# Kernel optimization log

Hardware: AMD Instinct MI355X
Metric: run time of the kernel (lower is better)

Reference implementation:

```python
import jax, jax.numpy as jnp
import numpy as np

B, T, D, NW, NC, S, L, H, FF = 32, 128, 512, 2000, 200, 8, 4, 8, 2048
HD = D // H


def layer_norm(x, g, b, eps=1e-5):
    m = jnp.mean(x, -1, keepdims=True)
    v = jnp.var(x, -1, keepdims=True)
    return (x - m) * jax.lax.rsqrt(v + eps) * g + b


def mha(x, Wq, bq, Wk, bk, Wv, bv, Wo, bo):
    b_, t_, d_ = x.shape
    q = (x @ Wq + bq).reshape(b_, t_, H, HD)
    k = (x @ Wk + bk).reshape(b_, t_, H, HD)
    v = (x @ Wv + bv).reshape(b_, t_, H, HD)
    s = jnp.einsum('bqhd,bkhd->bhqk', q, k) / np.float32(np.sqrt(HD))
    a = jax.nn.softmax(s, -1)
    o = jnp.einsum('bhqk,bkhd->bqhd', a, v).reshape(b_, t_, d_)
    return o @ Wo + bo


def conv1d(x, w, b):  # x [B,C,T], w [O,I,3], same padding
    y = jax.lax.conv_general_dilated(x, w, (1,), [(1, 1)], dimension_numbers=('NCH', 'OIH', 'NCH'))
    return y + b[None, :, None]


def setup_inputs() -> dict:
    key = jax.random.key(0)
    ks = jax.random.split(key, 48)
    n = lambda k, shape, s=0.02: jax.random.normal(k, shape, jnp.float32) * s
    inp = {}
    inp['vid_feats'] = jax.random.normal(ks[0], (B, T, D), jnp.float32)
    inp['segs_feats'] = jax.random.normal(ks[1], (B, S, D), jnp.float32)
    inp['actn_feats'] = jax.random.normal(ks[2], (NC, D), jnp.float32)
    inp['actn_concepts'] = jax.random.normal(ks[3], (NW, D), jnp.float32)
    inp['pos_enc'] = n(ks[4], (1, T, D))
    # TemporalTransformer (L stacked encoder layers, post-norm, relu FFN)
    inp['tf_Wq'] = n(ks[5], (L, D, D)); inp['tf_bq'] = jnp.zeros((L, D), jnp.float32)
    inp['tf_Wk'] = n(ks[6], (L, D, D)); inp['tf_bk'] = jnp.zeros((L, D), jnp.float32)
    inp['tf_Wv'] = n(ks[7], (L, D, D)); inp['tf_bv'] = jnp.zeros((L, D), jnp.float32)
    inp['tf_Wo'] = n(ks[8], (L, D, D)); inp['tf_bo'] = jnp.zeros((L, D), jnp.float32)
    inp['tf_W1'] = n(ks[9], (L, D, FF)); inp['tf_b1'] = jnp.zeros((L, FF), jnp.float32)
    inp['tf_W2'] = n(ks[10], (L, FF, D)); inp['tf_b2'] = jnp.zeros((L, D), jnp.float32)
    inp['tf_ln1_g'] = jnp.ones((L, D), jnp.float32); inp['tf_ln1_b'] = jnp.zeros((L, D), jnp.float32)
    inp['tf_ln2_g'] = jnp.ones((L, D), jnp.float32); inp['tf_ln2_b'] = jnp.zeros((L, D), jnp.float32)
    # AttentionProjectionModule (out_proj is defined but unused in its forward)
    inp['pq_W'] = n(ks[11], (D, D)); inp['pq_b'] = jnp.zeros((D,), jnp.float32)
    inp['pk_W'] = n(ks[12], (D, D)); inp['pk_b'] = jnp.zeros((D,), jnp.float32)
    inp['pv_W'] = n(ks[13], (D, D)); inp['pv_b'] = jnp.zeros((D,), jnp.float32)
    # temp_conv stack 2000->1024->512->256->128->1, k=3, pad=1
    inp['c1_w'] = n(ks[14], (1024, NW, 3)); inp['c1_b'] = jnp.zeros((1024,), jnp.float32)
    inp['c2_w'] = n(ks[15], (512, 1024, 3)); inp['c2_b'] = jnp.zeros((512,), jnp.float32)
    inp['c3_w'] = n(ks[16], (256, 512, 3)); inp['c3_b'] = jnp.zeros((256,), jnp.float32)
    inp['c4_w'] = n(ks[17], (128, 256, 3)); inp['c4_b'] = jnp.zeros((128,), jnp.float32)
    inp['c5_w'] = n(ks[18], (1, 128, 3)); inp['c5_b'] = jnp.zeros((1,), jnp.float32)
    # ragged segments: inclusive [start, end] per the torch stf:edf+1 slicing
    st = jax.random.randint(ks[19], (B, S), 0, T - 16)
    ln = jax.random.randint(ks[20], (B, S), 0, 16)
    ed = jnp.minimum(st + ln, T - 1)
    inp['seg_steds'] = jnp.stack([st, ed], -1).astype(jnp.int32)  # [B,S,2]
    return inp


def reference(vid_feats, segs_feats, actn_feats, actn_concepts, pos_enc,
              tf_Wq, tf_bq, tf_Wk, tf_bk, tf_Wv, tf_bv, tf_Wo, tf_bo,
              tf_W1, tf_b1, tf_W2, tf_b2, tf_ln1_g, tf_ln1_b, tf_ln2_g, tf_ln2_b,
              pq_W, pq_b, pk_W, pk_b, pv_W, pv_b,
              c1_w, c1_b, c2_w, c2_b, c3_w, c3_b, c4_w, c4_b, c5_w, c5_b,
              seg_steds):
    # --- TemporalTransformer ---
    x = vid_feats + pos_enc
    for l in range(L):
        x = layer_norm(x + mha(x, tf_Wq[l], tf_bq[l], tf_Wk[l], tf_bk[l], tf_Wv[l], tf_bv[l], tf_Wo[l], tf_bo[l]), tf_ln1_g[l], tf_ln1_b[l])
        ff = jax.nn.relu(x @ tf_W1[l] + tf_b1[l]) @ tf_W2[l] + tf_b2[l]
        x = layer_norm(x + ff, tf_ln2_g[l], tf_ln2_b[l])
    vid_feats_proj = vid_feats + x  # [B,T,D]
    # --- AttentionProjectionModule (words attend to video frames) ---
    wf = jax.lax.stop_gradient(actn_concepts)  # detached concept table [NW,D]
    Q = (wf @ pq_W + pq_b).reshape(NW, H, HD)  # shared across batch
    K = (vid_feats_proj @ pk_W + pk_b).reshape(B, T, H, HD)
    V = (vid_feats_proj @ pv_W + pv_b).reshape(B, T, H, HD)
    s = jnp.einsum('nhd,bthd->bhnt', Q, K) / np.float32(np.sqrt(HD))
    a = jax.nn.softmax(s, -1)
    upd = jnp.einsum('bhnt,bthd->bnhd', a, V).reshape(B, NW, D)
    feats_proj = jnp.einsum('btd,bnd->btn', vid_feats_proj, upd)  # [B,T,NW]
    # --- temp_conv + sigmoid ---
    h = feats_proj.transpose(0, 2, 1)  # [B,NW,T]
    h = jax.nn.relu(conv1d(h, c1_w, c1_b))
    h = jax.nn.relu(conv1d(h, c2_w, c2_b))
    h = jax.nn.relu(conv1d(h, c3_w, c3_b))
    h = jax.nn.relu(conv1d(h, c4_w, c4_b))
    frames_cls = jax.nn.sigmoid(conv1d(h, c5_w, c5_b))  # [B,1,T]
    weights = frames_cls[:, 0, :]  # [B,T]
    # --- ragged per-segment softmax-weighted sum pooling (mask-vectorized) ---
    t_idx = jnp.arange(T)
    st = seg_steds[..., 0]; ed = seg_steds[..., 1]  # [B,S]
    mask = (t_idx[None, None, :] >= st[..., None]) & (t_idx[None, None, :] <= ed[..., None])  # [B,S,T]
    scores = jnp.where(mask, weights[:, None, :], -1e30)
    w = jax.nn.softmax(scores, -1)  # per-segment softmax over frames in segment
    seg_feats = jnp.einsum('bst,btd->bsd', w, vid_feats)  # [B,S,D]
    actn_logits = jnp.einsum('bsd,cd->bsc', seg_feats, jax.lax.stop_gradient(actn_feats))  # [B,S,NC]
    return frames_cls, actn_logits, feats_proj
```

## Files before the change

### kernel.cpp

```cpp
#include <hip/hip_runtime.h>
#include <hip/hip_bf16.h>

#define BB 32
#define TT 128
#define DD 512
#define NW 2000
#define NCC 200
#define SS 8
#define LL 4
#define HH 8
#define FF 2048
#define HD 64

typedef unsigned short ushort_t;
typedef __attribute__((ext_vector_type(8))) short bhalf8;
typedef __attribute__((ext_vector_type(4))) float floatx4;

__device__ inline ushort_t f2b(float x) {
    union { float f; unsigned int u; } v; v.f = x;
    unsigned int r = (v.u + 0x7FFFu + ((v.u >> 16) & 1u)) >> 16;
    return (ushort_t)r;
}
__device__ inline float b2f(ushort_t u) {
    union { unsigned int u; float f; } v; v.u = ((unsigned int)u) << 16;
    return v.f;
}
__device__ inline void gld16(const ushort_t* g, ushort_t* l) {
    __builtin_amdgcn_global_load_lds(
        (const __attribute__((address_space(1))) void*)g,
        (__attribute__((address_space(3))) void*)l, 16, 0, 0);
}

template<int ACT, int OUTBF>
__global__ __launch_bounds__(256) void bgemm_k(
    const ushort_t* __restrict__ A, int lda, long sA1, long sA2,
    const ushort_t* __restrict__ B, int ldb, long sB1, long sB2,
    void* __restrict__ Cv, int ldc, long sC1, long sC2,
    const float* __restrict__ bias,
    int M, int N, int K, float alpha, int batchH,
    int taps, long tapA, long tapB, const ushort_t* __restrict__ zbuf)
{
    __shared__ __align__(16) ushort_t sm[2][2][128 * 64];
    int z = blockIdx.z;
    int zb = z / batchH, zh = z % batchH;
    A += (long)zb * sA1 + (long)zh * sA2;
    B += (long)zb * sB1 + (long)zh * sB2;
    long cOff = (long)zb * sC1 + (long)zh * sC2;
    int m0 = blockIdx.y * 128, n0 = blockIdx.x * 128;
    int tid = threadIdx.x;
    int wid = tid >> 6, lane = tid & 63;
    int wr = wid >> 1, wc = wid & 1;
    int lr = lane & 15, lg = lane >> 4;

    int kSteps = (K + 63) >> 6;
    int nt = taps * kSteps;

    int rsub = lane >> 3;
    int ssub = lane & 7;
    int scol = ((ssub ^ rsub) << 3);
    bool aok[4], bok[4];
    const ushort_t* aptr[4];
    const ushort_t* bptr[4];
    #pragma unroll
    for (int i = 0; i < 4; i++) {
        int row = (wid << 5) + (i << 3) + rsub;
        aok[i] = (m0 + row) < M;
        bok[i] = (n0 + row) < N;
        aptr[i] = A + (long)(m0 + row) * lda + scol;
        bptr[i] = B + (long)(n0 + row) * ldb + scol;
    }

    floatx4 acc[4][4];
    #pragma unroll
    for (int i = 0; i < 4; i++)
        #pragma unroll
        for (int j = 0; j < 4; j++)
            acc[i][j] = (floatx4){0.f, 0.f, 0.f, 0.f};

    {
        bool kOk = scol < K;
        #pragma unroll
        for (int i = 0; i < 4; i++) {
            const ushort_t* as = (kOk && aok[i]) ? aptr[i] : zbuf;
            const ushort_t* bs = (kOk && bok[i]) ? bptr[i] : zbuf;
            int lb = ((wid << 5) + (i << 3)) << 6;
            gld16(as, &sm[0][0][lb]);
            gld16(bs, &sm[0][1][lb]);
        }
    }
    __syncthreads();

    int cur = 0;
    int tap_n = 0, k0_n = 0;
    for (int t = 0; t < nt; t++) {
        k0_n += 64;
        if (k0_n >= K) { k0_n = 0; ++tap_n; }
        if (tap_n < taps) {
            bool kOk = (k0_n + scol) < K;
            #pragma unroll
            for (int i = 0; i < 4; i++) {
                const ushort_t* as =
                    (kOk && aok[i]) ? (aptr[i] + (long)tap_n * tapA + k0_n) : zbuf;
                const ushort_t* bs =
                    (kOk && bok[i]) ? (bptr[i] + (long)tap_n * tapB + k0_n) : zbuf;
                int lb = ((wid << 5) + (i << 3)) << 6;
                gld16(as, &sm[cur ^ 1][0][lb]);
                gld16(bs, &sm[cur ^ 1][1][lb]);
            }
        }
        const char* Ab = (const char*)&sm[cur][0][0];
        const char* Bbs = (const char*)&sm[cur][1][0];
        #pragma unroll
        for (int kk = 0; kk < 2; kk++) {
            bhalf8 a_[4], b_[4];
            #pragma unroll
            for (int i = 0; i < 4; i++) {
                int r = wr * 64 + i * 16 + lr;
                int off = (r << 7) + (((kk << 6) + (lg << 4)) ^ ((r & 7) << 4));
                a_[i] = *(const bhalf8*)(Ab + off);
            }
            #pragma unroll
            for (int j = 0; j < 4; j++) {
                int r = wc * 64 + j * 16 + lr;
                int off = (r << 7) + (((kk << 6) + (lg << 4)) ^ ((r & 7) << 4));
                b_[j] = *(const bhalf8*)(Bbs + off);
            }
            #pragma unroll
            for (int i = 0; i < 4; i++)
                #pragma unroll
                for (int j = 0; j < 4; j++)
                    acc[i][j] = __builtin_amdgcn_mfma_f32_16x16x32_bf16(
                        a_[i], b_[j], acc[i][j], 0, 0, 0);
        }
        __syncthreads();
        cur ^= 1;
    }

    #pragma unroll
    for (int i = 0; i < 4; i++) {
        int gm_base = m0 + wr * 64 + i * 16 + lg * 4;
        #pragma unroll
        for (int j = 0; j < 4; j++) {
            int gn = n0 + wc * 64 + j * 16 + lr;
            if (gn >= N) continue;
            float bv = bias ? bias[gn] : 0.f;
            #pragma unroll
            for (int r = 0; r < 4; r++) {
                int gm = gm_base + r;
                if (gm >= M) continue;
                float v = acc[i][j][r] * alpha + bv;
                if (ACT == 1) v = fmaxf(v, 0.f);
                long idx = cOff + (long)gm * ldc + gn;
                if (OUTBF) ((ushort_t*)Cv)[idx] = f2b(v);
                else       ((float*)Cv)[idx] = v;
            }
        }
    }
}

static void launch_bgemm(int act, int outbf,
                         const ushort_t* A, int lda, long sA1, long sA2,
                         const ushort_t* B, int ldb, long sB1, long sB2,
                         void* C, int ldc, long sC1, long sC2,
                         const float* bias, int M, int N, int K, float alpha,
                         int batchH, int Z, int taps, long tapA, long tapB,
                         const ushort_t* zbuf, hipStream_t st) {
    dim3 grid((N + 127) / 128, (M + 127) / 128, Z), blk(256);
#define BG(A_, O_) bgemm_k<A_, O_><<<grid, blk, 0, st>>>(A, lda, sA1, sA2, B, ldb, sB1, sB2, C, ldc, sC1, sC2, bias, M, N, K, alpha, batchH, taps, tapA, tapB, zbuf)
    if (act) { if (outbf) BG(1, 1); else BG(1, 0); }
    else     { if (outbf) BG(0, 1); else BG(0, 0); }
#undef BG
}

template<int CHECKQ>
__global__ __launch_bounds__(256) void fattn_k(
    const ushort_t* __restrict__ Q, int ldq, long sQb, long sQc,
    const ushort_t* __restrict__ K, int ldk, long sKb,
    const ushort_t* __restrict__ VT, long sVb,
    ushort_t* __restrict__ O, int ldo, long sOb, long sOc,
    int nc, int Mtot, const ushort_t* __restrict__ zbuf)
{
    __shared__ __align__(16) ushort_t Qs[128 * 64];
    __shared__ __align__(16) ushort_t Ks[128 * 64];
    __shared__ __align__(16) ushort_t Vs[64 * 128];
    __shared__ __align__(16) ushort_t Ps[128 * 128];
    int z = blockIdx.x;
    int c = z % nc, rr_ = z / nc;
    int h = rr_ % HH, b = rr_ / HH;
    int mQ = Mtot - c * 128;
    const ushort_t* Qb = Q + (long)b * sQb + (long)c * sQc + h * 64;
    const ushort_t* Kb = K + (long)b * sKb + h * 64;
    const ushort_t* Vb = VT + (long)b * sVb + (long)h * 64 * 128;
    ushort_t* Ob = O + (long)b * sOb + (long)c * sOc + h * 64;

    int tid = threadIdx.x, wid = tid >> 6, lane = tid & 63;
    int lr = lane & 15, lg = lane >> 4;

    {
        int rsub = lane >> 3, csub = lane & 7;
        #pragma unroll
        for (int i = 0; i < 4; i++) {
            int row = wid * 32 + i * 8 + rsub;
            int cc = (csub ^ rsub) * 8;
            const ushort_t* qs = (!CHECKQ || row < mQ) ? (Qb + (long)row * ldq + cc) : zbuf;
            gld16(qs, &Qs[(wid * 32 + i * 8) * 64]);
            gld16(Kb + (long)row * ldk + cc, &Ks[(wid * 32 + i * 8) * 64]);
        }
        int d4 = lane >> 4, c16 = lane & 15;
        #pragma unroll
        for (int i = 0; i < 4; i++) {
            int d = wid * 16 + i * 4 + d4;
            int cc = (c16 ^ (d & 7)) * 8;
            gld16(Vb + (long)d * 128 + cc, &Vs[(wid * 16 + i * 4) * 128]);
        }
    }
    __syncthreads();

    floatx4 acc[2][8];
    #pragma unroll
    for (int i = 0; i < 2; i++)
        #pragma unroll
        for (int j = 0; j < 8; j++)
            acc[i][j] = (floatx4){0.f, 0.f, 0.f, 0.f};
    const char* Qc = (const char*)Qs;
    const char* Kc = (const char*)Ks;
    #pragma unroll
    for (int kk = 0; kk < 2; kk++) {
        bhalf8 a_[2], b_[8];
        #pragma unroll
        for (int i = 0; i < 2; i++) {
            int r = wid * 32 + i * 16 + lr;
            a_[i] = *(const bhalf8*)(Qc + (r << 7) + ((((kk << 2) + lg) ^ (r & 7)) << 4));
        }
        #pragma unroll
        for (int j = 0; j < 8; j++) {
            int r = j * 16 + lr;
            b_[j] = *(const bhalf8*)(Kc + (r << 7) + ((((kk << 2) + lg) ^ (r & 7)) << 4));
        }
        #pragma unroll
        for (int i = 0; i < 2; i++)
            #pragma unroll
            for (int j = 0; j < 8; j++)
                acc[i][j] = __builtin_amdgcn_mfma_f32_16x16x32_bf16(
                    a_[i], b_[j], acc[i][j], 0, 0, 0);
    }

    #pragma unroll
    for (int i = 0; i < 2; i++) {
        #pragma unroll
        for (int r = 0; r < 4; r++) {
            int row = wid * 32 + i * 16 + lg * 4 + r;
            float v[8], m = -1e30f;
            #pragma unroll
            for (int j = 0; j < 8; j++) { v[j] = acc[i][j][r] * 0.125f; m = fmaxf(m, v[j]); }
            #pragma unroll
            for (int o = 8; o > 0; o >>= 1) m = fmaxf(m, __shfl_xor(m, o, 64));
            float s = 0.f;
            #pragma unroll
            for (int j = 0; j < 8; j++) { v[j] = expf(v[j] - m); s += v[j]; }
            #pragma unroll
            for (int o = 8; o > 0; o >>= 1) s += __shfl_xor(s, o, 64);
            float inv = 1.f / s;
            #pragma unroll
            for (int j = 0; j < 8; j++) {
                int col = j * 16 + lr;
                int byte = (row << 8) + ((((col >> 3) ^ (row & 7)) << 4)) + ((col & 7) << 1);
                *(ushort_t*)((char*)Ps + byte) = f2b(v[j] * inv);
            }
        }
    }
    __syncthreads();

    floatx4 acc2[2][4];
    #pragma unroll
    for (int i = 0; i < 2; i++)
        #pragma unroll
        for (int j = 0; j < 4; j++)
            acc2[i][j] = (floatx4){0.f, 0.f, 0.f, 0.f};
    const char* Pc = (const char*)Ps;
    const char* Vc = (const char*)Vs;
    #pragma unroll
    for (int kk = 0; kk < 4; kk++) {
        bhalf8 a_[2], b_[4];
        #pragma unroll
        for (int i = 0; i < 2; i++) {
            int r = wid * 32 + i * 16 + lr;
            a_[i] = *(const bhalf8*)(Pc + (r << 8) + ((((kk << 2) + lg) ^ (r & 7)) << 4));
        }
        #pragma unroll
        for (int j = 0; j < 4; j++) {
            int d = j * 16 + lr;
            b_[j] = *(const bhalf8*)(Vc + (d << 8) + ((((kk << 2) + lg) ^ (d & 7)) << 4));
        }
        #pragma unroll
        for (int i = 0; i < 2; i++)
            #pragma unroll
            for (int j = 0; j < 4; j++)
                acc2[i][j] = __builtin_amdgcn_mfma_f32_16x16x32_bf16(
                    a_[i], b_[j], acc2[i][j], 0, 0, 0);
    }
    #pragma unroll
    for (int i = 0; i < 2; i++) {
        #pragma unroll
        for (int r = 0; r < 4; r++) {
            int q = wid * 32 + i * 16 + lg * 4 + r;
            if (CHECKQ && q >= mQ) continue;
            #pragma unroll
            for (int j = 0; j < 4; j++) {
                int d = j * 16 + lr;
                Ob[(long)q * ldo + d] = f2b(acc2[i][j][r]);
            }
        }
    }
}

template<int TRANSB>
__global__ __launch_bounds__(256) void gemm_k(
    const float* __restrict__ A, int lda,
    const float* __restrict__ B, int ldb,
    float* __restrict__ C, int ldc,
    int M, int N, int K)
{
    __shared__ float As[16][68];
    __shared__ float Bs[16][68];
    int m0 = blockIdx.y * 64, n0 = blockIdx.x * 64;
    int tid = threadIdx.x;
    int tr = tid / 16, tc = tid % 16;
    float acc[4][4] = {};
    for (int k0 = 0; k0 < K; k0 += 16) {
        {
            int ar = tid / 4;
            int ac = (tid % 4) * 4;
            int gm = m0 + ar;
            #pragma unroll
            for (int i = 0; i < 4; i++) {
                int gk = k0 + ac + i;
                As[ac + i][ar] = (gm < M && gk < K) ? A[(long)gm * lda + gk] : 0.f;
            }
        }
        {
            int bn = tid / 4;
            int bk = (tid % 4) * 4;
            int gn = n0 + bn;
            #pragma unroll
            for (int i = 0; i < 4; i++) {
                int gk = k0 + bk + i;
                Bs[bk + i][bn] = (gn < N && gk < K) ? B[(long)gn * ldb + gk] : 0.f;
            }
        }
        __syncthreads();
        #pragma unroll
        for (int kk = 0; kk < 16; kk++) {
            float a[4], b[4];
            #pragma unroll
            for (int i = 0; i < 4; i++) a[i] = As[kk][tr * 4 + i];
            #pragma unroll
            for (int i = 0; i < 4; i++) b[i] = Bs[kk][tc * 4 + i];
            #pragma unroll
            for (int i = 0; i < 4; i++)
                #pragma unroll
                for (int j = 0; j < 4; j++)
                    acc[i][j] += a[i] * b[j];
        }
        __syncthreads();
    }
    #pragma unroll
    for (int i = 0; i < 4; i++) {
        int gm = m0 + tr * 4 + i;
        if (gm >= M) continue;
        #pragma unroll
        for (int j = 0; j < 4; j++) {
            int gn = n0 + tc * 4 + j;
            if (gn >= N) continue;
            C[(long)gm * ldc + gn] = acc[i][j];
        }
    }
}

__global__ void f2b_k(const float* __restrict__ in, ushort_t* __restrict__ out, long n) {
    long stride = (long)gridDim.x * blockDim.x * 8;
    for (long i = ((long)blockIdx.x * blockDim.x + threadIdx.x) * 8; i < n; i += stride) {
        float4 a = *(const float4*)(in + i);
        float4 b = *(const float4*)(in + i + 4);
        uint4 o;
        o.x = (unsigned)f2b(a.x) | ((unsigned)f2b(a.y) << 16);
        o.y = (unsigned)f2b(a.z) | ((unsigned)f2b(a.w) << 16);
        o.z = (unsigned)f2b(b.x) | ((unsigned)f2b(b.y) << 16);
        o.w = (unsigned)f2b(b.z) | ((unsigned)f2b(b.w) << 16);
        *(uint4*)(out + i) = o;
    }
}
__global__ void add_f2b_k(const float* __restrict__ a, const float* __restrict__ b,
                          ushort_t* __restrict__ out, long n) {
    long stride = (long)gridDim.x * blockDim.x * 8;
    for (long i = ((long)blockIdx.x * blockDim.x + threadIdx.x) * 8; i < n; i += stride) {
        float4 x = *(const float4*)(a + i);
        float4 y = *(const float4*)(b + i);
        float4 x2 = *(const float4*)(a + i + 4);
        float4 y2 = *(const float4*)(b + i + 4);
        uint4 o;
        o.x = (unsigned)f2b(x.x + y.x) | ((unsigned)f2b(x.y + y.y) << 16);
        o.y = (unsigned)f2b(x.z + y.z) | ((unsigned)f2b(x.w + y.w) << 16);
        o.z = (unsigned)f2b(x2.x + y2.x) | ((unsigned)f2b(x2.y + y2.y) << 16);
        o.w = (unsigned)f2b(x2.z + y2.z) | ((unsigned)f2b(x2.w + y2.w) << 16);
        *(uint4*)(out + i) = o;
    }
}
__global__ void f2b_t_k(const float* __restrict__ in, ushort_t* __restrict__ out,
                        int R, int C, long inStride, long outStride) {
    __shared__ float tile[32][33];
    int z = blockIdx.z;
    in += (long)z * inStride;
    out += (long)z * outStride;
    int c0 = blockIdx.x * 32, r0 = blockIdx.y * 32;
    int tx = threadIdx.x, ty = threadIdx.y;
    #pragma unroll
    for (int i = 0; i < 32; i += 8) {
        int r = r0 + ty + i, c = c0 + tx;
        tile[ty + i][tx] = (r < R && c < C) ? in[(long)r * C + c] : 0.f;
    }
    __syncthreads();
    #pragma unroll
    for (int i = 0; i < 32; i += 8) {
        int c = c0 + ty + i, r = r0 + tx;
        if (c < C && r < R) out[(long)c * R + r] = f2b(tile[tx][ty + i]);
    }
}
__global__ void t_bf_k(const ushort_t* __restrict__ in, ushort_t* __restrict__ out,
                       int R, int C, int ldin, long inStride, long outStride) {
    __shared__ ushort_t tile[32][33];
    int z = blockIdx.z;
    in += (long)z * inStride;
    out += (long)z * outStride;
    int c0 = blockIdx.x * 32, r0 = blockIdx.y * 32;
    int tx = threadIdx.x, ty = threadIdx.y;
    #pragma unroll
    for (int i = 0; i < 32; i += 8) {
        int r = r0 + ty + i, c = c0 + tx;
        if (r < R && c < C) tile[ty + i][tx] = in[(long)r * ldin + c];
    }
    __syncthreads();
    #pragma unroll
    for (int i = 0; i < 32; i += 8) {
        int c = c0 + ty + i, r = r0 + tx;
        if (c < C && r < R) out[(long)c * R + r] = tile[tx][ty + i];
    }
}
__global__ void cat3all_k(float* __restrict__ dst, const float* __restrict__ a,
                          const float* __restrict__ b, const float* __restrict__ c) {
    int i = blockIdx.x * blockDim.x + threadIdx.x;
    if (i >= LL * 1536) return;
    int l = i / 1536, j = i % 1536;
    float v = (j < 512) ? a[l * 512 + j]
            : (j < 1024) ? b[l * 512 + j - 512] : c[l * 512 + j - 1024];
    dst[i] = v;
}

__global__ void addpos_bf_k(const float* __restrict__ a, const float* __restrict__ pos,
                            float* __restrict__ o, ushort_t* __restrict__ obf,
                            long n, long pmod) {
    for (long i = blockIdx.x * (long)blockDim.x + threadIdx.x; i < n;
         i += (long)gridDim.x * blockDim.x) {
        float v = a[i] + pos[i % pmod];
        o[i] = v;
        obf[i] = f2b(v);
    }
}
__global__ void zero_k(float* __restrict__ p, long n) {
    for (long i = blockIdx.x * (long)blockDim.x + threadIdx.x; i < n;
         i += (long)gridDim.x * blockDim.x)
        p[i] = 0.f;
}
__global__ void sentinel_k(float* p) { p[0] = 1e9f; }
__global__ void padzero_k(ushort_t* __restrict__ h, int CO) {
    int b = blockIdx.x;
    for (int i = threadIdx.x; i < CO; i += blockDim.x) {
        h[(long)b * 130 * CO + i] = 0;
        h[((long)b * 130 + 129) * CO + i] = 0;
    }
}

__global__ __launch_bounds__(256) void ln_res_k(float* __restrict__ x,
                                                const float* __restrict__ z,
                                                ushort_t* __restrict__ xbf,
                                                const float* __restrict__ g,
                                                const float* __restrict__ b) {
    long row = blockIdx.x;
    float* px = x + row * DD;
    const float* pz = z + row * DD;
    ushort_t* pb = xbf + row * DD;
    int t = threadIdx.x;
    float v0 = px[t] + pz[t];
    float v1 = px[t + 256] + pz[t + 256];
    float s = v0 + v1, sq = v0 * v0 + v1 * v1;
    for (int o = 32; o > 0; o >>= 1) {
        s += __shfl_xor(s, o, 64);
        sq += __shfl_xor(sq, o, 64);
    }
    __shared__ float ss[4], sqq[4];
    int wave = t >> 6, lane = t & 63;
    if (lane == 0) { ss[wave] = s; sqq[wave] = sq; }
    __syncthreads();
    s = ss[0] + ss[1] + ss[2] + ss[3];
    sq = sqq[0] + sqq[1] + sqq[2] + sqq[3];
    float mean = s * (1.f / DD);
    float var = sq * (1.f / DD) - mean * mean;
    float rstd = 1.f / sqrtf(var + 1e-5f);
    float o0 = (v0 - mean) * rstd * g[t] + b[t];
    float o1 = (v1 - mean) * rstd * g[t + 256] + b[t + 256];
    px[t] = o0;
    px[t + 256] = o1;
    pb[t] = f2b(o0);
    pb[t + 256] = f2b(o1);
}

__global__ void pad_copy_bf_k(const float* __restrict__ fp, ushort_t* __restrict__ fpp) {
    long total = (long)BB * TT * NW;
    for (long i = blockIdx.x * (long)blockDim.x + threadIdx.x; i < total;
         i += (long)gridDim.x * blockDim.x) {
        long ci = i % NW;
        long r = i / NW;
        long t = r % TT;
        long b = r / TT;
        fpp[(b * 130 + t + 1) * NW + ci] = f2b(fp[i]);
    }
}
__global__ void repack_bf_k(const float* __restrict__ w, ushort_t* __restrict__ wk,
                            int CO, int CI) {
    long total = (long)CO * CI * 3;
    for (long i = blockIdx.x * (long)blockDim.x + threadIdx.x; i < total;
         i += (long)gridDim.x * blockDim.x) {
        long kt = i % 3;
        long r = i / 3;
        long ci = r % CI;
        long co = r / CI;
        wk[kt * (long)CO * CI + co * CI + ci] = f2b(w[i]);
    }
}
__global__ __launch_bounds__(128) void conv5_bf_k(const ushort_t* __restrict__ h4,
                                                  const float* __restrict__ w,
                                                  const float* __restrict__ bias,
                                                  float* __restrict__ out) {
    int b = blockIdx.x, t = threadIdx.x;
    __shared__ float wsm[384];
    wsm[t] = w[t];
    wsm[t + 128] = w[t + 128];
    wsm[t + 256] = w[t + 256];
    __syncthreads();
    const ushort_t* hb = h4 + (long)b * 130 * 128;
    float acc = bias[0];
    for (int ci = 0; ci < 128; ci++) {
        float w0 = wsm[ci * 3], w1 = wsm[ci * 3 + 1], w2 = wsm[ci * 3 + 2];
        acc += w0 * b2f(hb[(t + 0) * 128 + ci]) + w1 * b2f(hb[(t + 1) * 128 + ci]) +
               w2 * b2f(hb[(t + 2) * 128 + ci]);
    }
    out[b * TT + t] = 1.f / (1.f + expf(-acc));
}

__global__ __launch_bounds__(128) void seg_pool_k(const float* __restrict__ weights,
                                                  const int* __restrict__ steds,
                                                  const float* __restrict__ vid,
                                                  float* __restrict__ segf) {
    int b = blockIdx.y, sidx = blockIdx.x;
    int st = steds[(b * SS + sidx) * 2];
    int ed = steds[(b * SS + sidx) * 2 + 1];
    int t = threadIdx.x;
    float w = (t >= st && t <= ed) ? weights[b * TT + t] : -1e30f;
    __shared__ float red[2];
    __shared__ float aw[TT];
    int wave = t >> 6, lane = t & 63;
    float m = w;
    for (int o = 32; o > 0; o >>= 1) m = fmaxf(m, __shfl_xor(m, o, 64));
    if (lane == 0) red[wave] = m;
    __syncthreads();
    m = fmaxf(red[0], red[1]);
    float e = expf(w - m);
    float sum = e;
    for (int o = 32; o > 0; o >>= 1) sum += __shfl_xor(sum, o, 64);
    __syncthreads();
    if (lane == 0) red[wave] = sum;
    __syncthreads();
    sum = red[0] + red[1];
    aw[t] = e / sum;
    __syncthreads();
    #pragma unroll
    for (int i = 0; i < 4; i++) {
        int d = t + i * 128;
        float acc = 0.f;
        for (int tt = 0; tt < TT; tt++)
            acc += aw[tt] * vid[((long)b * TT + tt) * DD + d];
        segf[((long)b * SS + sidx) * DD + d] = acc;
    }
}

extern "C" void kernel_launch(void* const* d_in, const int* in_sizes, int n_in,
                              void* d_out, int out_size, void* d_ws, size_t ws_size,
                              hipStream_t stream) {
    const float* vid = (const float*)d_in[0];
    const float* actn_feats = (const float*)d_in[2];
    const float* actn_concepts = (const float*)d_in[3];
    const float* pos = (const float*)d_in[4];
    const float* Wq = (const float*)d_in[5];
    const float* bq = (const float*)d_in[6];
    const float* Wk = (const float*)d_in[7];
    const float* bk = (const float*)d_in[8];
    const float* Wv = (const float*)d_in[9];
    const float* bv = (const float*)d_in[10];
    const float* Wo = (const float*)d_in[11];
    const float* bo = (const float*)d_in[12];
    const float* W1 = (const float*)d_in[13];
    const float* b1 = (const float*)d_in[14];
    const float* W2 = (const float*)d_in[15];
    const float* b2 = (const float*)d_in[16];
    const float* g1 = (const float*)d_in[17];
    const float* bb1 = (const float*)d_in[18];
    const float* g2 = (const float*)d_in[19];
    const float* bb2 = (const float*)d_in[20];
    const float* pqW = (const float*)d_in[21];
    const float* pqb = (const float*)d_in[22];
    const float* pkW = (const float*)d_in[23];
    const float* pkb = (const float*)d_in[24];
    const float* pvW = (const float*)d_in[25];
    const float* pvb = (const float*)d_in[26];
    const float* c1w = (const float*)d_in[27];
    const float* c1b = (const float*)d_in[28];
    const float* c2w = (const float*)d_in[29];
    const float* c2b = (const float*)d_in[30];
    const float* c3w = (const float*)d_in[31];
    const float* c3b = (const float*)d_in[32];
    const float* c4w = (const float*)d_in[33];
    const float* c4b = (const float*)d_in[34];
    const float* c5w = (const float*)d_in[35];
    const float* c5b = (const float*)d_in[36];
    const int* steds = (const int*)d_in[37];

    float* out = (float*)d_out;
    float* fc_out = out;
    float* al_out = out + 4096;
    float* fp_out = out + 55296;

    float* ws = (float*)d_ws;
    const long NEED = 25165824;
    if (ws_size < (size_t)NEED * 4) {
        sentinel_k<<<1, 1, 0, stream>>>(fc_out);
        return;
    }

    const long A_XBF   = 0;
    const long A_QKVBF = 1048576;
    const long A_VT    = 4194304;
    const long A_FFH   = 7340032;
    const long A_AOBF  = 11534336;
    const long A_QB    = 12582912;
    const long A_QKVT  = 14680064;
    const long A_WOT   = 16252928;
    const long A_W1T   = 16777216;
    const long A_W2T   = 18874368;
    const long A_QKVB  = 20971520;
    const long XB      = 21000192;
    const long B_UPD   = 0;
    const long B_VPRBF = 16384000;
    const long B_PW    = 17432576;
    const long B_ACBF  = 17825792;
    const long B_QPBF  = 18337792;
    const long B_KPBF  = 18849792;
    const long B_VP    = 19898368;
    const long B_VPT   = 21995520;
    const long C_FPP   = 0;
    const long C_WK1   = 4160000;
    const long C_WK2   = 7232000;
    const long C_WK3   = 8018432;
    const long C_WK4   = 8215040;
    const long C_H1    = 8264192;
    const long C_H2    = 10394112;
    const long C_H3    = 11459072;
    const long C_H4    = 11991552;
    const long C_SEGF  = 12257792;
    const long ZPAD    = 25165760;

    float* xb = ws + XB;
    const ushort_t* zbuf = (const ushort_t*)(ws + ZPAD);
    const long nBTD = (long)BB * TT * DD;

    zero_k<<<1, 64, 0, stream>>>(ws + ZPAD, 64);

    ushort_t* xbf = (ushort_t*)(ws + A_XBF);
    addpos_bf_k<<<2048, 256, 0, stream>>>(vid, pos, xb, xbf, nBTD, (long)TT * DD);

    ushort_t* qkvT = (ushort_t*)(ws + A_QKVT);
    ushort_t* WoT  = (ushort_t*)(ws + A_WOT);
    ushort_t* W1T  = (ushort_t*)(ws + A_W1T);
    ushort_t* W2T  = (ushort_t*)(ws + A_W2T);
    float*    qkvb = ws + A_QKVB;
    dim3 tblk(32, 8);
    f2b_t_k<<<dim3(16, 16, LL), tblk, 0, stream>>>(Wq, qkvT, DD, DD, (long)DD * DD, 786432);
    f2b_t_k<<<dim3(16, 16, LL), tblk, 0, stream>>>(Wk, qkvT + 262144, DD, DD, (long)DD * DD, 786432);
    f2b_t_k<<<dim3(16, 16, LL), tblk, 0, stream>>>(Wv, qkvT + 524288, DD, DD, (long)DD * DD, 786432);
    f2b_t_k<<<dim3(16, 16, LL), tblk, 0, stream>>>(Wo, WoT, DD, DD, (long)DD * DD, 262144);
    f2b_t_k<<<dim3(64, 16, LL), tblk, 0, stream>>>(W1, W1T, DD, FF, (long)DD * FF, 1048576);
    f2b_t_k<<<dim3(16, 64, LL), tblk, 0, stream>>>(W2, W2T, FF, DD, (long)FF * DD, 1048576);
    cat3all_k<<<(LL * 1536 + 255) / 256, 256, 0, stream>>>(qkvb, bq, bk, bv);

    ushort_t* qkvbf = (ushort_t*)(ws + A_QKVBF);
    ushort_t* vTb   = (ushort_t*)(ws + A_VT);
    ushort_t* ffhbf = (ushort_t*)(ws + A_FFH);
    ushort_t* aobf  = (ushort_t*)(ws + A_AOBF);
    float*    qb    = ws + A_QB;

    for (int l = 0; l < LL; l++) {
        launch_bgemm(0, 1, xbf, DD, 0, 0, qkvT + (long)l * 786432, DD, 0, 0,
                     qkvbf, 1536, 0, 0, qkvb + (long)l * 1536,
                     BB * TT, 1536, DD, 1.f, 1, 1, 1, 0, 0, zbuf, stream);
        t_bf_k<<<dim3(16, 4, BB), tblk, 0, stream>>>(qkvbf + 1024, vTb, TT, DD, 1536,
                                                     (long)TT * 1536, (long)DD * TT);
        fattn_k<0><<<BB * HH, 256, 0, stream>>>(
            qkvbf, 1536, (long)TT * 1536, 0,
            qkvbf + 512, 1536, (long)TT * 1536,
            vTb, (long)DD * TT,
            aobf, DD, (long)TT * DD, 0, 1, TT, zbuf);
        launch_bgemm(0, 0, aobf, DD, 0, 0, WoT + (long)l * 262144, DD, 0, 0,
                     qb, DD, 0, 0, bo + (long)l * DD,
                     BB * TT, DD, DD, 1.f, 1, 1, 1, 0, 0, zbuf, stream);
        ln_res_k<<<BB * TT, 256, 0, stream>>>(xb, qb, xbf, g1 + (long)l * DD, bb1 + (long)l * DD);
        launch_bgemm(1, 1, xbf, DD, 0, 0, W1T + (long)l * 1048576, DD, 0, 0,
                     ffhbf, FF, 0, 0, b1 + (long)l * FF,
                     BB * TT, FF, DD, 1.f, 1, 1, 1, 0, 0, zbuf, stream);
        launch_bgemm(0, 0, ffhbf, FF, 0, 0, W2T + (long)l * 1048576, FF, 0, 0,
                     qb, DD, 0, 0, b2 + (long)l * DD,
                     BB * TT, DD, FF, 1.f, 1, 1, 1, 0, 0, zbuf, stream);
        ln_res_k<<<BB * TT, 256, 0, stream>>>(xb, qb, xbf, g2 + (long)l * DD, bb2 + (long)l * DD);
    }

    ushort_t* updbf = (ushort_t*)(ws + B_UPD);
    ushort_t* vprbf = (ushort_t*)(ws + B_VPRBF);
    ushort_t* pqT   = (ushort_t*)(ws + B_PW);
    ushort_t* pkT   = (ushort_t*)(ws + B_PW + 131072);
    ushort_t* pvT   = (ushort_t*)(ws + B_PW + 262144);
    ushort_t* acbf  = (ushort_t*)(ws + B_ACBF);
    ushort_t* Qpbf  = (ushort_t*)(ws + B_QPBF);
    ushort_t* Kpbf  = (ushort_t*)(ws + B_KPBF);
    float*    Vp    = ws + B_VP;
    ushort_t* VpT   = (ushort_t*)(ws + B_VPT);

    add_f2b_k<<<1024, 256, 0, stream>>>(vid, xb, vprbf, nBTD);
    f2b_t_k<<<dim3(16, 16, 1), tblk, 0, stream>>>(pqW, pqT, DD, DD, 0, 0);
    f2b_t_k<<<dim3(16, 16, 1), tblk, 0, stream>>>(pkW, pkT, DD, DD, 0, 0);
    f2b_t_k<<<dim3(16, 16, 1), tblk, 0, stream>>>(pvW, pvT, DD, DD, 0, 0);
    f2b_k<<<512, 256, 0, stream>>>(actn_concepts, acbf, (long)NW * DD);

    launch_bgemm(0, 1, acbf, DD, 0, 0, pqT, DD, 0, 0, Qpbf, DD, 0, 0,
                 pqb, NW, DD, DD, 1.f, 1, 1, 1, 0, 0, zbuf, stream);
    launch_bgemm(0, 1, vprbf, DD, 0, 0, pkT, DD, 0, 0, Kpbf, DD, 0, 0,
                 pkb, BB * TT, DD, DD, 1.f, 1, 1, 1, 0, 0, zbuf, stream);
    launch_bgemm(0, 0, vprbf, DD, 0, 0, pvT, DD, 0, 0, Vp, DD, 0, 0,
                 pvb, BB * TT, DD, DD, 1.f, 1, 1, 1, 0, 0, zbuf, stream);
    f2b_t_k<<<dim3(16, 4, BB), tblk, 0, stream>>>(Vp, VpT, TT, DD, (long)TT * DD, (long)TT * DD);

    fattn_k<1><<<BB * HH * 16, 256, 0, stream>>>(
        Qpbf, DD, 0, (long)128 * DD,
        Kpbf, DD, (long)TT * DD,
        VpT, (long)DD * TT,
        updbf, DD, (long)NW * DD, (long)128 * DD, 16, NW, zbuf);

    launch_bgemm(0, 0, vprbf, DD, (long)TT * DD, 0,
                 updbf, DD, (long)NW * DD, 0,
                 fp_out, NW, (long)TT * NW, 0,
                 nullptr, TT, NW, DD, 1.f, 1, BB, 1, 0, 0, zbuf, stream);

    ushort_t* fpp = (ushort_t*)(ws + C_FPP);
    ushort_t* wk1 = (ushort_t*)(ws + C_WK1);
    ushort_t* wk2 = (ushort_t*)(ws + C_WK2);
    ushort_t* wk3 = (ushort_t*)(ws + C_WK3);
    ushort_t* wk4 = (ushort_t*)(ws + C_WK4);
    ushort_t* h1  = (ushort_t*)(ws + C_H1);
    ushort_t* h2  = (ushort_t*)(ws + C_H2);
    ushort_t* h3  = (ushort_t*)(ws + C_H3);
    ushort_t* h4  = (ushort_t*)(ws + C_H4);

    repack_bf_k<<<1024, 256, 0, stream>>>(c1w, wk1, 1024, NW);
    repack_bf_k<<<512, 256, 0, stream>>>(c2w, wk2, 512, 1024);
    repack_bf_k<<<256, 256, 0, stream>>>(c3w, wk3, 256, 512);
    repack_bf_k<<<128, 256, 0, stream>>>(c4w, wk4, 128, 256);
    padzero_k<<<BB, 256, 0, stream>>>(fpp, NW);
    pad_copy_bf_k<<<2048, 256, 0, stream>>>(fp_out, fpp);

    const int MROWS = BB * 130 - 2;
    launch_bgemm(1, 1, fpp, NW, 0, 0, wk1, NW, 0, 0,
                 h1 + 1024, 1024, 0, 0, c1b,
                 MROWS, 1024, NW, 1.f, 1, 1, 3, NW, (long)1024 * NW, zbuf, stream);
    padzero_k<<<BB, 256, 0, stream>>>(h1, 1024);
    launch_bgemm(1, 1, h1, 1024, 0, 0, wk2, 1024, 0, 0,
                 h2 + 512, 512, 0, 0, c2b,
                 MROWS, 512, 1024, 1.f, 1, 1, 3, 1024, (long)512 * 1024, zbuf, stream);
    padzero_k<<<BB, 256, 0, stream>>>(h2, 512);
    launch_bgemm(1, 1, h2, 512, 0, 0, wk3, 512, 0, 0,
                 h3 + 256, 256, 0, 0, c3b,
                 MROWS, 256, 512, 1.f, 1, 1, 3, 512, (long)256 * 512, zbuf, stream);
    padzero_k<<<BB, 256, 0, stream>>>(h3, 256);
    launch_bgemm(1, 1, h3, 256, 0, 0, wk4, 256, 0, 0,
                 h4 + 128, 128, 0, 0, c4b,
                 MROWS, 128, 256, 1.f, 1, 1, 3, 256, (long)128 * 256, zbuf, stream);
    padzero_k<<<BB, 256, 0, stream>>>(h4, 128);
    conv5_bf_k<<<BB, 128, 0, stream>>>(h4, c5w, c5b, fc_out);

    float* segf = ws + C_SEGF;
    seg_pool_k<<<dim3(SS, BB), 128, 0, stream>>>(fc_out, steds, vid, segf);
    gemm_k<1><<<dim3((NCC + 63) / 64, (BB * SS + 63) / 64, 1), 256, 0, stream>>>(
        segf, DD, actn_feats, DD, al_out, NCC, BB * SS, NCC, DD);
}
```

Measured before the change: 1.235 ms.

## Split-K GEMMs for small-N projections and conv layers with fused reduction

Several GEMMs with few output tiles are split along K into 2 or 4 batched partial planes so more workgroups run at once. A new kred_k kernel sums the planes and applies bias, ReLU and bf16 conversion. The Wo and W2 GEMMs instead sum their partials inside the layernorm-residual kernel. This trades extra fp32 partial writes and reads for higher GPU occupancy on tile-starved GEMMs.

After: 1.294 ms. 1.05x slower.

```diff
diff --git a/kernel.cpp b/kernel.cpp
--- a/kernel.cpp
+++ b/kernel.cpp
@@ -172,6 +172,36 @@
 #undef BG
 }
 
+template<int OUTBF, int ACT>
+__global__ void kred_k(const float* __restrict__ p, long plane, int ks,
+                       const float* __restrict__ bias, int N,
+                       void* __restrict__ out, long total) {
+    long stride = (long)gridDim.x * blockDim.x * 4;
+    for (long i = ((long)blockIdx.x * blockDim.x + threadIdx.x) * 4; i < total;
+         i += stride) {
+        float4 v = *(const float4*)(p + i);
+        for (int s = 1; s < ks; s++) {
+            float4 w = *(const float4*)(p + s * plane + i);
+            v.x += w.x; v.y += w.y; v.z += w.z; v.w += w.w;
+        }
+        int co = (int)(i % N);
+        float4 bv = *(const float4*)(bias + co);
+        v.x += bv.x; v.y += bv.y; v.z += bv.z; v.w += bv.w;
+        if (ACT == 1) {
+            v.x = fmaxf(v.x, 0.f); v.y = fmaxf(v.y, 0.f);
+            v.z = fmaxf(v.z, 0.f); v.w = fmaxf(v.w, 0.f);
+        }
+        if (OUTBF) {
+            uint2 o;
+            o.x = (unsigned)f2b(v.x) | ((unsigned)f2b(v.y) << 16);
+            o.y = (unsigned)f2b(v.z) | ((unsigned)f2b(v.w) << 16);
+            *(uint2*)((ushort_t*)out + i) = o;
+        } else {
+            *(float4*)((float*)out + i) = v;
+        }
+    }
+}
+
 template<int CHECKQ>
 __global__ __launch_bounds__(256) void fattn_k(
     const ushort_t* __restrict__ Q, int ldq, long sQb, long sQc,
@@ -480,18 +510,20 @@
     }
 }
 
-__global__ __launch_bounds__(256) void ln_res_k(float* __restrict__ x,
-                                                const float* __restrict__ z,
-                                                ushort_t* __restrict__ xbf,
-                                                const float* __restrict__ g,
-                                                const float* __restrict__ b) {
+__global__ __launch_bounds__(256) void ln_res2_k(float* __restrict__ x,
+                                                 const float* __restrict__ p,
+                                                 long plane,
+                                                 const float* __restrict__ bias,
+                                                 ushort_t* __restrict__ xbf,
+                                                 const float* __restrict__ g,
+                                                 const float* __restrict__ b) {
     long row = blockIdx.x;
     float* px = x + row * DD;
-    const float* pz = z + row * DD;
+    const float* pp = p + row * DD;
     ushort_t* pb = xbf + row * DD;
     int t = threadIdx.x;
-    float v0 = px[t] + pz[t];
-    float v1 = px[t + 256] + pz[t + 256];
+    float v0 = px[t] + pp[t] + pp[t + plane] + bias[t];
+    float v1 = px[t + 256] + pp[t + 256] + pp[t + 256 + plane] + bias[t + 256];
     float s = v0 + v1, sq = v0 * v0 + v1 * v1;
     for (int o = 32; o > 0; o >>= 1) {
         s += __shfl_xor(s, o, 64);
@@ -649,15 +681,16 @@
     const long A_XBF   = 0;
     const long A_QKVBF = 1048576;
     const long A_VT    = 4194304;
+    const long A_PL    = 1048576;
     const long A_FFH   = 7340032;
     const long A_AOBF  = 11534336;
-    const long A_QB    = 12582912;
     const long A_QKVT  = 14680064;
     const long A_WOT   = 16252928;
     const long A_W1T   = 16777216;
     const long A_W2T   = 18874368;
     const long A_QKVB  = 20971520;
     const long XB      = 21000192;
+    const long B_PL    = 0;
     const long B_UPD   = 0;
     const long B_VPRBF = 16384000;
     const long B_PW    = 17432576;
@@ -676,6 +709,7 @@
     const long C_H3    = 11459072;
     const long C_H4    = 11991552;
     const long C_SEGF  = 12257792;
+    const long C_PBUF  = 12390400;
     const long ZPAD    = 25165760;
 
     float* xb = ws + XB;
@@ -705,7 +739,8 @@
     ushort_t* vTb   = (ushort_t*)(ws + A_VT);
     ushort_t* ffhbf = (ushort_t*)(ws + A_FFH);
     ushort_t* aobf  = (ushort_t*)(ws + A_AOBF);
-    float*    qb    = ws + A_QB;
+    float*    apl   = ws + A_PL;
+    const long APLANE = (long)BB * TT * DD;
 
     for (int l = 0; l < LL; l++) {
         launch_bgemm(0, 1, xbf, DD, 0, 0, qkvT + (long)l * 786432, DD, 0, 0,
@@ -718,20 +753,23 @@
             qkvbf + 512, 1536, (long)TT * 1536,
             vTb, (long)DD * TT,
             aobf, DD, (long)TT * DD, 0, 1, TT, zbuf);
-        launch_bgemm(0, 0, aobf, DD, 0, 0, WoT + (long)l * 262144, DD, 0, 0,
-                     qb, DD, 0, 0, bo + (long)l * DD,
-                     BB * TT, DD, DD, 1.f, 1, 1, 1, 0, 0, zbuf, stream);
-        ln_res_k<<<BB * TT, 256, 0, stream>>>(xb, qb, xbf, g1 + (long)l * DD, bb1 + (long)l * DD);
+        launch_bgemm(0, 0, aobf, DD, 256, 0, WoT + (long)l * 262144, DD, 256, 0,
+                     apl, DD, APLANE, 0, nullptr,
+                     BB * TT, DD, 256, 1.f, 1, 2, 1, 0, 0, zbuf, stream);
+        ln_res2_k<<<BB * TT, 256, 0, stream>>>(xb, apl, APLANE, bo + (long)l * DD,
+                                               xbf, g1 + (long)l * DD, bb1 + (long)l * DD);
         launch_bgemm(1, 1, xbf, DD, 0, 0, W1T + (long)l * 1048576, DD, 0, 0,
                      ffhbf, FF, 0, 0, b1 + (long)l * FF,
                      BB * TT, FF, DD, 1.f, 1, 1, 1, 0, 0, zbuf, stream);
-        launch_bgemm(0, 0, ffhbf, FF, 0, 0, W2T + (long)l * 1048576, FF, 0, 0,
-                     qb, DD, 0, 0, b2 + (long)l * DD,
-                     BB * TT, DD, FF, 1.f, 1, 1, 1, 0, 0, zbuf, stream);
-        ln_res_k<<<BB * TT, 256, 0, stream>>>(xb, qb, xbf, g2 + (long)l * DD, bb2 + (long)l * DD);
+        launch_bgemm(0, 0, ffhbf, FF, 1024, 0, W2T + (long)l * 1048576, FF, 1024, 0,
+                     apl, DD, APLANE, 0, nullptr,
+                     BB * TT, DD, 1024, 1.f, 1, 2, 1, 0, 0, zbuf, stream);
+        ln_res2_k<<<BB * TT, 256, 0, stream>>>(xb, apl, APLANE, b2 + (long)l * DD,
+                                               xbf, g2 + (long)l * DD, bb2 + (long)l * DD);
     }
 
     ushort_t* updbf = (ushort_t*)(ws + B_UPD);
+    float*    bpl   = ws + B_PL;
     ushort_t* vprbf = (ushort_t*)(ws + B_VPRBF);
     ushort_t* pqT   = (ushort_t*)(ws + B_PW);
     ushort_t* pkT   = (ushort_t*)(ws + B_PW + 131072);
@@ -748,12 +786,27 @@
     f2b_t_k<<<dim3(16, 16, 1), tblk, 0, stream>>>(pvW, pvT, DD, DD, 0, 0);
     f2b_k<<<512, 256, 0, stream>>>(actn_concepts, acbf, (long)NW * DD);
 
-    launch_bgemm(0, 1, acbf, DD, 0, 0, pqT, DD, 0, 0, Qpbf, DD, 0, 0,
-                 pqb, NW, DD, DD, 1.f, 1, 1, 1, 0, 0, zbuf, stream);
-    launch_bgemm(0, 1, vprbf, DD, 0, 0, pkT, DD, 0, 0, Kpbf, DD, 0, 0,
-                 pkb, BB * TT, DD, DD, 1.f, 1, 1, 1, 0, 0, zbuf, stream);
-    launch_bgemm(0, 0, vprbf, DD, 0, 0, pvT, DD, 0, 0, Vp, DD, 0, 0,
-                 pvb, BB * TT, DD, DD, 1.f, 1, 1, 1, 0, 0, zbuf, stream);
+    {
+        long plane = (long)NW * DD;
+        launch_bgemm(0, 0, acbf, DD, 256, 0, pqT, DD, 256, 0,
+                     bpl, DD, plane, 0, nullptr,
+                     NW, DD, 256, 1.f, 1, 2, 1, 0, 0, zbuf, stream);
+        kred_k<1, 0><<<1024, 256, 0, stream>>>(bpl, plane, 2, pqb, DD, Qpbf, plane);
+    }
+    {
+        long plane = nBTD;
+        launch_bgemm(0, 0, vprbf, DD, 256, 0, pkT, DD, 256, 0,
+                     bpl, DD, plane, 0, nullptr,
+                     BB * TT, DD, 256, 1.f, 1, 2, 1, 0, 0, zbuf, stream);
+        kred_k<1, 0><<<1024, 256, 0, stream>>>(bpl, plane, 2, pkb, DD, Kpbf, plane);
+    }
+    {
+        long plane = nBTD;
+        launch_bgemm(0, 0, vprbf, DD, 256, 0, pvT, DD, 256, 0,
+                     bpl, DD, plane, 0, nullptr,
+                     BB * TT, DD, 256, 1.f, 1, 2, 1, 0, 0, zbuf, stream);
+        kred_k<0, 0><<<1024, 256, 0, stream>>>(bpl, plane, 2, pvb, DD, Vp, plane);
+    }
     f2b_t_k<<<dim3(16, 4, BB), tblk, 0, stream>>>(Vp, VpT, TT, DD, (long)TT * DD, (long)TT * DD);
 
     fattn_k<1><<<BB * HH * 16, 256, 0, stream>>>(
@@ -776,6 +829,7 @@
     ushort_t* h2  = (ushort_t*)(ws + C_H2);
     ushort_t* h3  = (ushort_t*)(ws + C_H3);
     ushort_t* h4  = (ushort_t*)(ws + C_H4);
+    float*    pbuf = ws + C_PBUF;
 
     repack_bf_k<<<1024, 256, 0, stream>>>(c1w, wk1, 1024, NW);
     repack_bf_k<<<512, 256, 0, stream>>>(c2w, wk2, 512, 1024);
@@ -785,21 +839,37 @@
     pad_copy_bf_k<<<2048, 256, 0, stream>>>(fp_out, fpp);
 
     const int MROWS = BB * 130 - 2;
-    launch_bgemm(1, 1, fpp, NW, 0, 0, wk1, NW, 0, 0,
-                 h1 + 1024, 1024, 0, 0, c1b,
-                 MROWS, 1024, NW, 1.f, 1, 1, 3, NW, (long)1024 * NW, zbuf, stream);
+    {
+        long plane = (long)MROWS * 1024;
+        launch_bgemm(0, 0, fpp, NW, 1000, 0, wk1, NW, 1000, 0,
+                     pbuf, 1024, plane, 0, nullptr,
+                     MROWS, 1024, 1000, 1.f, 1, 2, 3, NW, (long)1024 * NW, zbuf, stream);
+        kred_k<1, 1><<<2048, 256, 0, stream>>>(pbuf, plane, 2, c1b, 1024, h1 + 1024, plane);
+    }
     padzero_k<<<BB, 256, 0, stream>>>(h1, 1024);
-    launch_bgemm(1, 1, h1, 1024, 0, 0, wk2, 1024, 0, 0,
-                 h2 + 512, 512, 0, 0, c2b,
-                 MROWS, 512, 1024, 1.f, 1, 1, 3, 1024, (long)512 * 1024, zbuf, stream);
+    {
+        long plane = (long)MROWS * 512;
+        launch_bgemm(0, 0, h1, 1024, 512, 0, wk2, 1024, 512, 0,
+                     pbuf, 512, plane, 0, nullptr,
+                     MROWS, 512, 512, 1.f, 1, 2, 3, 1024, (long)512 * 1024, zbuf, stream);
+        kred_k<1, 1><<<2048, 256, 0, stream>>>(pbuf, plane, 2, c2b, 512, h2 + 512, plane);
+    }
     padzero_k<<<BB, 256, 0, stream>>>(h2, 512);
-    launch_bgemm(1, 1, h2, 512, 0, 0, wk3, 512, 0, 0,
-                 h3 + 256, 256, 0, 0, c3b,
-                 MROWS, 256, 512, 1.f, 1, 1, 3, 512, (long)256 * 512, zbuf, stream);
+    {
+        long plane = (long)MROWS * 256;
+        launch_bgemm(0, 0, h2, 512, 128, 0, wk3, 512, 128, 0,
+                     pbuf, 256, plane, 0, nullptr,
+                     MROWS, 256, 128, 1.f, 1, 4, 3, 512, (long)256 * 512, zbuf, stream);
+        kred_k<1, 1><<<1024, 256, 0, stream>>>(pbuf, plane, 4, c3b, 256, h3 + 256, plane);
+    }
     padzero_k<<<BB, 256, 0, stream>>>(h3, 256);
-    launch_bgemm(1, 1, h3, 256, 0, 0, wk4, 256, 0, 0,
-                 h4 + 128, 128, 0, 0, c4b,
-                 MROWS, 128, 256, 1.f, 1, 1, 3, 256, (long)128 * 256, zbuf, stream);
+    {
+        long plane = (long)MROWS * 128;
+        launch_bgemm(0, 0, h3, 256, 64, 0, wk4, 256, 64, 0,
+                     pbuf, 128, plane, 0, nullptr,
+                     MROWS, 128, 64, 1.f, 1, 4, 3, 256, (long)128 * 256, zbuf, stream);
+        kred_k<1, 1><<<512, 256, 0, stream>>>(pbuf, plane, 4, c4b, 128, h4 + 128, plane);
+    }
     padzero_k<<<BB, 256, 0, stream>>>(h4, 128);
     conv5_bf_k<<<BB, 128, 0, stream>>>(h4, c5w, c5b, fc_out);
 
```
